# Performance work log

Hardware: AMD Instinct MI355X
Metric: run time of the kernel (lower is better)

The kernel has to match this reference:

```python
import jax, jax.numpy as jnp
import numpy as np

DIM = 1024
HEADS = 8
DIM_HEAD = 64
INNER = HEADS * DIM_HEAD  # 512
N_PATCHES = 256
SCALE = DIM_HEAD ** -0.5


def setup_inputs() -> dict:
    key = jax.random.key(0)
    ks = jax.random.split(key, 6)
    s = lambda fan_in: 1.0 / np.sqrt(fan_in)
    return {
        "x": jax.random.normal(ks[0], (64, N_PATCHES, DIM), dtype=jnp.float32),
        "Wq": jax.random.normal(ks[1], (DIM, INNER), dtype=jnp.float32) * s(DIM),
        "Wkv": jax.random.normal(ks[2], (DIM, 2 * INNER), dtype=jnp.float32) * s(DIM),
        "Wout": jax.random.normal(ks[3], (INNER, DIM), dtype=jnp.float32) * s(INNER),
        "bout": jax.random.normal(ks[4], (DIM,), dtype=jnp.float32) * 0.01,
        "Wspec": jax.random.normal(ks[5], (N_PATCHES, 3 * N_PATCHES), dtype=jnp.float32) * s(N_PATCHES),
    }


def reference(x, Wq, Wkv, Wout, bout, Wspec):
    b, n, d = x.shape
    # ---- spatial: single center-query attention ----
    x_center = x[:, n // 2, :]                      # [b, d]
    q = (x_center @ Wq).reshape(b, HEADS, DIM_HEAD)  # [b, h, dh]
    kv = x @ Wkv                                     # [b, n, 2*inner]
    k, v = jnp.split(kv, 2, axis=-1)
    k = k.reshape(b, n, HEADS, DIM_HEAD).transpose(0, 2, 1, 3)  # [b, h, n, dh]
    v = v.reshape(b, n, HEADS, DIM_HEAD).transpose(0, 2, 1, 3)
    logits = jnp.einsum('bhd,bhnd->bhn', q, k) * SCALE
    attn = jax.nn.softmax(logits, axis=-1)           # [b, h, n]
    out = jnp.einsum('bhn,bhnd->bhd', attn, v).reshape(b, INNER)
    # torch expands attn over n identical rows BEFORE to_out; the rows are
    # identical, so broadcasting the projected row is the same math.
    spatial = out @ Wout + bout                      # [b, d]
    spatial_out = jnp.broadcast_to(spatial[:, None, :], (b, n, d))
    # ---- spectral: attention over transposed (feature) axis ----
    x_t = x.transpose(0, 2, 1)                       # [b, d, n]
    qkv = x_t @ Wspec                                # [b, d, 3n]
    q_s, k_s, v_s = jnp.split(qkv, 3, axis=-1)       # v_s unused (as in source)
    spec_logits = jnp.einsum('bin,bjn->bij', q_s, k_s) * SCALE  # [b, d, d]
    spec_weights = jax.nn.softmax(spec_logits, axis=-1)
    return jnp.einsum('bnd,bde->bne', spatial_out, spec_weights)
```

## Files before the change

### kernel.cpp

```cpp
#include <hip/hip_runtime.h>
#include <hip/hip_bf16.h>
#include <cstdint>

typedef _Float16 f16;
typedef _Float16 half8 __attribute__((ext_vector_type(8)));
typedef float f32x4 __attribute__((ext_vector_type(4)));

#define SCALE 0.125f

#define GLL(src, dst) __builtin_amdgcn_global_load_lds( \
    (const __attribute__((address_space(1))) unsigned int*)(src), \
    (__attribute__((address_space(3))) unsigned int*)(dst), 16, 0, 0)

__global__ __launch_bounds__(256) void prep_xT(const float* __restrict__ x, f16* __restrict__ xT) {
  __shared__ f16 tile[32][33];
  int b = blockIdx.z, nt = blockIdx.y, dt = blockIdx.x;
  int c = threadIdx.x & 31, rp = threadIdx.x >> 5;
  const float* xb = x + ((size_t)b*256 + nt*32)*1024 + dt*32;
#pragma unroll
  for (int p = 0; p < 4; ++p) { int r = p*8 + rp; tile[r][c] = (f16)xb[(size_t)r*1024 + c]; }
  __syncthreads();
  f16* o = xT + ((size_t)b*1024 + dt*32)*256 + nt*32;
#pragma unroll
  for (int p = 0; p < 4; ++p) { int r = p*8 + rp; o[(size_t)r*256 + c] = tile[c][r]; }
}

__global__ __launch_bounds__(256) void prep_WspecT(const float* __restrict__ W, f16* __restrict__ Wt) {
  __shared__ float tile[32][33];
  int jt = blockIdx.x, ct = blockIdx.y;
  int c = threadIdx.x & 31, rp = threadIdx.x >> 5;
#pragma unroll
  for (int p = 0; p < 4; ++p) { int r = p*8+rp; tile[r][c] = W[(size_t)(ct*32 + r)*768 + jt*32 + c]; }
  __syncthreads();
#pragma unroll
  for (int p = 0; p < 4; ++p) { int r = p*8+rp; Wt[(size_t)(jt*32 + r)*256 + ct*32 + c] = (f16)tile[c][r]; }
}

template<int KSTEPS, int AST, int BST, int CST, bool SCALEQ>
__global__ __launch_bounds__(256) void gemm128(const f16* __restrict__ Ag, const f16* __restrict__ Bg,
                                               f16* __restrict__ Cg, size_t aB, size_t bB, size_t cB) {
  __shared__ f16 As[2][128*32];
  __shared__ f16 Bs[2][128*32];
  const f16* A = Ag + (size_t)blockIdx.z*aB;
  const f16* B = Bg + (size_t)blockIdx.z*bB;
  f16* C = Cg + (size_t)blockIdx.z*cB;
  int t = threadIdx.x, lane = t & 63, wave = t >> 6;
  int l15 = lane & 15, l4 = lane >> 4;
  int wm = wave & 1, wn = wave >> 1;
  size_t m0 = (size_t)blockIdx.x*128, n0 = (size_t)blockIdx.y*128;
  float cscale = (SCALEQ && n0 < 256) ? SCALE : 1.0f;
  f32x4 acc[4][4];
#pragma unroll
  for (int i=0;i<4;++i)
#pragma unroll
    for (int j=0;j<4;++j) acc[i][j] = (f32x4){0.f,0.f,0.f,0.f};
  int rowS[2], chS[2];
#pragma unroll
  for (int c=0;c<2;++c) {
    int slot = c*256 + t;
    rowS[c] = slot >> 2;
    chS[c]  = (slot & 3) ^ ((slot >> 3) & 3);
  }
  int pc = (l4 ^ ((l15 >> 1) & 3)) * 8;

  auto STAGE = [&](int buf, int ks) {
    int k0 = ks*32;
#pragma unroll
    for (int c=0;c<2;++c) {
      GLL(A + (m0 + rowS[c])*(size_t)AST + k0 + chS[c]*8, &As[buf][(c*256 + wave*64)*8]);
      GLL(B + (n0 + rowS[c])*(size_t)BST + k0 + chS[c]*8, &Bs[buf][(c*256 + wave*64)*8]);
    }
  };

  STAGE(0, 0);
#pragma unroll 2
  for (int ks = 0; ks < KSTEPS; ++ks) {
    int cur = ks & 1;
    if (ks + 1 < KSTEPS) {
      STAGE(cur ^ 1, ks + 1);
      asm volatile("s_waitcnt vmcnt(4)" ::: "memory");
    } else {
      asm volatile("s_waitcnt vmcnt(0)" ::: "memory");
    }
    __builtin_amdgcn_s_barrier();
    __builtin_amdgcn_sched_barrier(0);
    half8 a[4], bb[4];
    const f16* Af = &As[cur][(wm*64 + l15)*32 + pc];
    const f16* Bf = &Bs[cur][(wn*64 + l15)*32 + pc];
#pragma unroll
    for (int mi=0;mi<4;++mi) a[mi]  = *(const half8*)(Af + mi*16*32);
#pragma unroll
    for (int ni=0;ni<4;++ni) bb[ni] = *(const half8*)(Bf + ni*16*32);
    __builtin_amdgcn_s_setprio(1);
#pragma unroll
    for (int mi=0;mi<4;++mi)
#pragma unroll
      for (int ni=0;ni<4;++ni)
        acc[mi][ni] = __builtin_amdgcn_mfma_f32_16x16x32_f16(a[mi], bb[ni], acc[mi][ni], 0,0,0);
    __builtin_amdgcn_s_setprio(0);
    __builtin_amdgcn_sched_barrier(0);
    __builtin_amdgcn_s_barrier();
  }
#pragma unroll
  for (int mi=0;mi<4;++mi)
#pragma unroll
    for (int ni=0;ni<4;++ni)
#pragma unroll
      for (int j=0;j<4;++j) {
        size_t row = m0 + wm*64 + mi*16 + 4*l4 + j;
        size_t col = n0 + wn*64 + ni*16 + l15;
        C[row*CST + col] = (f16)(acc[mi][ni][j] * cscale);
      }
}

__global__ __launch_bounds__(256) void qk(const float* __restrict__ x, const float* __restrict__ Wq,
                                          float* __restrict__ qbuf) {
  int b = blockIdx.x, h = blockIdx.y;
  int t = threadIdx.x;
  __shared__ float xc[1024];
  __shared__ float part[4][64];
  const float* xcg = x + ((size_t)b*256 + 128)*1024;
#pragma unroll
  for (int i = 0; i < 4; ++i) xc[t + 256*i] = xcg[t + 256*i];
  __syncthreads();
  int d = t & 63, chunk = t >> 6;
  float s = 0.f;
  const float* wq = Wq + (size_t)(chunk*256)*512 + h*64 + d;
#pragma unroll 8
  for (int c = 0; c < 256; ++c) s += xc[chunk*256 + c] * wq[(size_t)c*512];
  part[chunk][d] = s;
  __syncthreads();
  if (t < 64) qbuf[(size_t)b*512 + h*64 + t] = part[0][t]+part[1][t]+part[2][t]+part[3][t];
}

__global__ __launch_bounds__(256) void uk(const float* __restrict__ Wkv, const float* __restrict__ qbuf,
                                          f16* __restrict__ u16) {
  int h = blockIdx.x, dc = blockIdx.y;
  int t = threadIdx.x;
  __shared__ float Wk[32][64];
  __shared__ float qT[64][65];
  {
    int j = t & 63, g = t >> 6;
#pragma unroll
    for (int rr = 0; rr < 8; ++rr) {
      int dd = g*8 + rr;
      Wk[dd][j] = Wkv[(size_t)(dc*32 + dd)*1024 + h*64 + j];
    }
#pragma unroll
    for (int rr = 0; rr < 16; ++rr) {
      int bb = g*16 + rr;
      qT[j][bb] = qbuf[(size_t)bb*512 + h*64 + j];
    }
  }
  __syncthreads();
  int b = t & 63, dq = t >> 6;
#pragma unroll
  for (int i = 0; i < 8; ++i) {
    int dd = dq*8 + i;
    float s = 0.f;
#pragma unroll 8
    for (int j = 0; j < 64; ++j) s += qT[j][b] * Wk[dd][j];
    u16[((size_t)b*16 + h)*1024 + dc*32 + dd] = (f16)s;
  }
}

__global__ __launch_bounds__(64) void lgk(const float* __restrict__ x, const f16* __restrict__ u16,
                                          float* __restrict__ logitbuf) {
  int mt = blockIdx.x, b = blockIdx.y;
  int lane = threadIdx.x, l15 = lane & 15, l4 = lane >> 4;
  const float* Ap = x + ((size_t)b*256 + mt*16 + l15)*1024 + 8*l4;
  const f16* Bp = u16 + ((size_t)b*16 + l15)*1024 + 8*l4;
  f32x4 acc = (f32x4){0.f,0.f,0.f,0.f};
#pragma unroll 8
  for (int ks = 0; ks < 32; ++ks) {
    f32x4 lo = *(const f32x4*)(Ap + ks*32);
    f32x4 hi = *(const f32x4*)(Ap + ks*32 + 4);
    half8 h;
    h[0]=(f16)lo[0]; h[1]=(f16)lo[1]; h[2]=(f16)lo[2]; h[3]=(f16)lo[3];
    h[4]=(f16)hi[0]; h[5]=(f16)hi[1]; h[6]=(f16)hi[2]; h[7]=(f16)hi[3];
    acc = __builtin_amdgcn_mfma_f32_16x16x32_f16(h, *(const half8*)(Bp + ks*32), acc, 0,0,0);
  }
  if (l15 < 8) {
#pragma unroll
    for (int j = 0; j < 4; ++j)
      logitbuf[((size_t)b*256 + mt*16 + 4*l4 + j)*8 + l15] = acc[j];
  }
}

__global__ __launch_bounds__(256) void sm(const float* __restrict__ logitbuf, f16* __restrict__ attnW) {
  int b = blockIdx.x, t = threadIdx.x;
  __shared__ float eL[256][9];
  __shared__ float Zs[8];
  float e[8];
  const float* lp = logitbuf + (size_t)b*256*8 + (size_t)t*8;
#pragma unroll
  for (int h = 0; h < 8; ++h) { e[h] = __expf(lp[h] * SCALE); eL[t][h] = e[h]; }
  __syncthreads();
  {
    int h = t >> 5, i = t & 31;
    float s = 0.f;
#pragma unroll
    for (int k = 0; k < 8; ++k) s += eL[i + 32*k][h];
#pragma unroll
    for (int o = 1; o < 32; o <<= 1) s += __shfl_xor(s, o);
    if (i == 0) Zs[h] = s;
  }
  __syncthreads();
#pragma unroll
  for (int h = 0; h < 8; ++h) attnW[((size_t)b*16 + h)*256 + t] = (f16)(e[h] / Zs[h]);
#pragma unroll
  for (int h = 8; h < 16; ++h) attnW[((size_t)b*16 + h)*256 + t] = (f16)0.f;
}

__global__ __launch_bounds__(64) void xbk(const f16* __restrict__ attnW, const f16* __restrict__ xT,
                                          f16* __restrict__ xbar) {
  int dt = blockIdx.x, b = blockIdx.y;
  int lane = threadIdx.x, l15 = lane & 15, l4 = lane >> 4;
  const f16* Ap = attnW + ((size_t)b*16 + l15)*256 + 8*l4;
  const f16* Bp = xT + ((size_t)b*1024 + dt*16 + l15)*256 + 8*l4;
  f32x4 acc = (f32x4){0.f,0.f,0.f,0.f};
#pragma unroll
  for (int ks = 0; ks < 8; ++ks)
    acc = __builtin_amdgcn_mfma_f32_16x16x32_f16(*(const half8*)(Ap + ks*32),
                                                 *(const half8*)(Bp + ks*32), acc, 0,0,0);
  if (l4 < 2) {
#pragma unroll
    for (int j = 0; j < 4; ++j)
      xbar[((size_t)b*8 + 4*l4 + j)*1024 + dt*16 + l15] = (f16)acc[j];
  }
}

__global__ __launch_bounds__(256) void vk(const f16* __restrict__ xbar, const float* __restrict__ Wkv,
                                          float* __restrict__ attnout) {
  int h = blockIdx.x, dc = blockIdx.y, bc = blockIdx.z;
  int t = threadIdx.x;
  __shared__ float Wv[256][64];
  {
    int j = t & 63, g = t >> 6;
#pragma unroll
    for (int rr = 0; rr < 64; ++rr) {
      int dd = g*64 + rr;
      Wv[dd][j] = Wkv[(size_t)(dc*256 + dd)*1024 + 512 + h*64 + j];
    }
  }
  __syncthreads();
  int j = t & 63, bq = t >> 6;
  float s[4] = {0.f,0.f,0.f,0.f};
  const f16* xp[4];
#pragma unroll
  for (int bl = 0; bl < 4; ++bl)
    xp[bl] = xbar + ((size_t)(bc*16 + bq*4 + bl)*8 + h)*1024 + dc*256;
  for (int d8 = 0; d8 < 32; ++d8) {
    half8 xv[4];
#pragma unroll
    for (int bl = 0; bl < 4; ++bl) xv[bl] = *(const half8*)(xp[bl] + d8*8);
#pragma unroll
    for (int i = 0; i < 8; ++i) {
      float w = Wv[d8*8 + i][j];
#pragma unroll
      for (int bl = 0; bl < 4; ++bl) s[bl] += (float)xv[bl][i] * w;
    }
  }
#pragma unroll
  for (int bl = 0; bl < 4; ++bl)
    atomicAdd(&attnout[(size_t)(bc*16 + bq*4 + bl)*512 + h*64 + j], s[bl]);
}

__global__ __launch_bounds__(256) void spatialp(const float* __restrict__ attnout, const float* __restrict__ Wout,
                                                float* __restrict__ partial) {
  int ic = blockIdx.x, b = blockIdx.y;
  int t = threadIdx.x;
  __shared__ float ao[128];
  if (t < 128) ao[t] = attnout[(size_t)b*512 + ic*128 + t];
  __syncthreads();
  const float* W = Wout + (size_t)ic*128*1024 + t*4;
  f32x4 acc0 = (f32x4){0.f,0.f,0.f,0.f};
  f32x4 acc1 = (f32x4){0.f,0.f,0.f,0.f};
#pragma unroll 4
  for (int i = 0; i < 128; i += 2) {
    f32x4 w0 = *(const f32x4*)(W + (size_t)i*1024);
    f32x4 w1 = *(const f32x4*)(W + (size_t)(i+1)*1024);
    float a0 = ao[i], a1 = ao[i+1];
    acc0[0] += a0*w0[0]; acc0[1] += a0*w0[1]; acc0[2] += a0*w0[2]; acc0[3] += a0*w0[3];
    acc1[0] += a1*w1[0]; acc1[1] += a1*w1[1]; acc1[2] += a1*w1[2]; acc1[3] += a1*w1[3];
  }
  f32x4 acc;
#pragma unroll
  for (int j=0;j<4;++j) acc[j] = acc0[j] + acc1[j];
  *(f32x4*)(partial + ((size_t)(b*4 + ic))*1024 + t*4) = acc;
}

__global__ __launch_bounds__(256) void spatialr(const float* __restrict__ partial, const float* __restrict__ bout,
                                                float* __restrict__ spatial) {
  int b = blockIdx.x, t = threadIdx.x;
  f32x4 s = *(const f32x4*)(bout + t*4);
#pragma unroll
  for (int ic = 0; ic < 4; ++ic) {
    f32x4 p = *(const f32x4*)(partial + ((size_t)(b*4 + ic))*1024 + t*4);
#pragma unroll
    for (int j=0;j<4;++j) s[j] += p[j];
  }
  *(f32x4*)(spatial + (size_t)b*1024 + t*4) = s;
}

__global__ __launch_bounds__(1024, 4) void speck(const f16* __restrict__ qks, const float* __restrict__ spatial,
                                                 float* __restrict__ r) {
  __shared__ f16 Bs[4][512*32];
  __shared__ f16 As[3][64*32];
  __shared__ __attribute__((aligned(16))) float sz[64*16];
  __shared__ float spat[64];
  __shared__ float zfin[64];
  int bid = blockIdx.x;
  int xcd = bid & 7, q = bid >> 3;
  int b = xcd*8 + (q >> 4);
  int iblk = q & 15;
  int t = threadIdx.x, lane = t & 63, wave = t >> 6;
  int l15 = lane & 15, l4 = lane >> 4;
  const f16* qs = qks + (size_t)b*1024*512;
  int i0 = iblk*64;
  if (t < 64) spat[t] = spatial[(size_t)b*1024 + i0 + t];

  f32x4 acc[4][4];
#pragma unroll
  for (int mi=0;mi<4;++mi)
#pragma unroll
    for (int ni=0;ni<4;++ni) acc[mi][ni] = (f32x4){0.f,0.f,0.f,0.f};
  int pc = (l4 ^ ((l15 >> 1) & 3)) * 8;

  auto STAGE = [&](int p) {
    int s = p & 3, hh = p & 1, ks = p >> 1;
    int k0 = ks*32;
#pragma unroll
    for (int c = 0; c < 2; ++c) {
      int u = c*1024 + t;
      int row = u >> 2;
      int ch = (u & 3) ^ ((u >> 3) & 3);
      GLL(qs + (size_t)(hh*512 + row)*512 + 256 + k0 + ch*8, &Bs[s][(c*1024 + wave*64)*8]);
    }
    if (hh == 0 && wave < 4) {
      int u = wave*64 + lane;
      int row = u >> 2;
      int ch = (u & 3) ^ ((u >> 3) & 3);
      GLL(qs + (size_t)(i0 + row)*512 + k0 + ch*8, &As[ks % 3][(wave*64)*8]);
    }
  };

  STAGE(0); STAGE(1); STAGE(2);
  half8 a[4];
#pragma unroll
  for (int p = 0; p < 16; ++p) {
    if (p < 14) {
      if (wave < 4) asm volatile("s_waitcnt vmcnt(5)" ::: "memory");
      else          asm volatile("s_waitcnt vmcnt(4)" ::: "memory");
    } else if (p == 14) {
      asm volatile("s_waitcnt vmcnt(2)" ::: "memory");
    } else {
      asm volatile("s_waitcnt vmcnt(0)" ::: "memory");
    }
    __builtin_amdgcn_s_barrier();
    __builtin_amdgcn_sched_barrier(0);
    if (p < 13) STAGE(p + 3);
    {
      int s = p & 3, hh = p & 1, sA = (p >> 1) % 3;
      if (hh == 0) {
#pragma unroll
        for (int mi = 0; mi < 4; ++mi)
          a[mi] = *(const half8*)(&As[sA][(mi*16 + l15)*32 + pc]);
      }
      __builtin_amdgcn_s_setprio(1);
#pragma unroll
      for (int c = 0; c < 2; ++c) {
        half8 bb = *(const half8*)(&Bs[s][(wave*32 + c*16 + l15)*32 + pc]);
#pragma unroll
        for (int mi = 0; mi < 4; ++mi)
          acc[mi][hh*2+c] = __builtin_amdgcn_mfma_f32_16x16x32_f16(a[mi], bb, acc[mi][hh*2+c], 0,0,0);
      }
      __builtin_amdgcn_s_setprio(0);
      __builtin_amdgcn_sched_barrier(0);
    }
  }
#pragma unroll
  for (int mi=0;mi<4;++mi)
#pragma unroll
    for (int jj=0;jj<4;++jj) {
      float s = 0.f;
#pragma unroll
      for (int ni=0;ni<4;++ni) {
        float e = __expf(acc[mi][ni][jj]);
        acc[mi][ni][jj] = e;
        s += e;
      }
#pragma unroll
      for (int o=1;o<16;o<<=1) s += __shfl_xor(s, o);
      if (l15 == 0) sz[(mi*16 + 4*l4 + jj)*16 + wave] = s;
    }
  __syncthreads();
  {
    float v = sz[t];
#pragma unroll
    for (int o=1;o<16;o<<=1) v += __shfl_xor(v, o);
    if ((t & 15) == 0) zfin[t >> 4] = v;
  }
  __syncthreads();
  float f[4][4];
#pragma unroll
  for (int mi=0;mi<4;++mi)
#pragma unroll
    for (int jj=0;jj<4;++jj) {
      int row = mi*16 + 4*l4 + jj;
      f[mi][jj] = spat[row] / zfin[row];
    }
  float* rb = r + (size_t)b*1024;
#pragma unroll
  for (int ni=0;ni<4;++ni) {
    float v = 0.f;
#pragma unroll
    for (int mi=0;mi<4;++mi)
#pragma unroll
      for (int jj=0;jj<4;++jj) v += f[mi][jj]*acc[mi][ni][jj];
    v += __shfl_xor(v, 16);
    v += __shfl_xor(v, 32);
    if (l4 == 0) atomicAdd(rb + (ni>>1)*512 + wave*32 + (ni&1)*16 + l15, v);
  }
}

__global__ __launch_bounds__(256) void bcast(const float* __restrict__ r, float* __restrict__ out) {
  size_t row = blockIdx.x;
  int b = (int)(row >> 8);
  f32x4 v = *(const f32x4*)(r + (size_t)b*1024 + threadIdx.x*4);
  *(f32x4*)(out + row*1024 + (size_t)threadIdx.x*4) = v;
}

extern "C" void kernel_launch(void* const* d_in, const int* in_sizes, int n_in,
                              void* d_out, int out_size, void* d_ws, size_t ws_size,
                              hipStream_t stream) {
  const float* x     = (const float*)d_in[0];
  const float* Wq    = (const float*)d_in[1];
  const float* Wkv   = (const float*)d_in[2];
  const float* Wout  = (const float*)d_in[3];
  const float* bout  = (const float*)d_in[4];
  const float* Wspec = (const float*)d_in[5];
  float* out = (float*)d_out;
  char* ws = (char*)d_ws;
  f16*   qks      = (f16*)(ws);
  f16*   u16pad   = (f16*)(ws);
  float* partial  = (float*)(ws);
  float* logitbuf = (float*)(ws + 2097152);
  f16*   attnW    = (f16*)(ws + 2621440);
  f16*   xbar     = (f16*)(ws + 3145728);
  float* qbuf     = (float*)(ws + 5242880);
  f16*   xT       = (f16*)(ws + 67108864);
  f16*   WspecT   = (f16*)(ws + 102760448);
  float* attnout  = (float*)(ws + 103022592);
  float* spatial  = (float*)(ws + 103153664);
  float* rvec     = (float*)(ws + 103415808);
  (void)in_sizes; (void)n_in; (void)out_size; (void)ws_size;

  prep_xT    <<<dim3(32, 8, 64), dim3(256), 0, stream>>>(x, xT);
  prep_WspecT<<<dim3(16, 8),     dim3(256), 0, stream>>>(Wspec, WspecT);
  hipMemsetAsync(u16pad, 0, 2097152, stream);
  hipMemsetAsync(attnout, 0, 64*512*sizeof(float), stream);
  qk         <<<dim3(64, 8),     dim3(256), 0, stream>>>(x, Wq, qbuf);
  uk         <<<dim3(8, 32),     dim3(256), 0, stream>>>(Wkv, qbuf, u16pad);
  lgk        <<<dim3(16, 64),    dim3(64),  0, stream>>>(x, u16pad, logitbuf);
  sm         <<<dim3(64),        dim3(256), 0, stream>>>(logitbuf, attnW);
  xbk        <<<dim3(64, 64),    dim3(64),  0, stream>>>(attnW, xT, xbar);
  vk         <<<dim3(8, 4, 4),   dim3(256), 0, stream>>>(xbar, Wkv, attnout);
  spatialp   <<<dim3(4, 64),     dim3(256), 0, stream>>>(attnout, Wout, partial);
  spatialr   <<<dim3(64),        dim3(256), 0, stream>>>(partial, bout, spatial);
  gemm128<8,256,256,512,true><<<dim3(8, 4, 64), dim3(256), 0, stream>>>(xT, WspecT, qks,
                                                                   (size_t)1024*256, 0, (size_t)1024*512);
  hipMemsetAsync(rvec, 0, 64*1024*sizeof(float), stream);
  speck      <<<dim3(1024),      dim3(1024), 0, stream>>>(qks, spatial, rvec);
  bcast      <<<dim3(16384),     dim3(256), 0, stream>>>(rvec, out);
}
```

Measured before the change: 223.4 us.

## Reassociate spectral logits through a precomputed Wq·Wkᵀ product

Rewrites the spectral logits q_s·k_sᵀ = xT·Wq_s·Wk_sᵀ·x as (xT·M)·x with M = Wq_s·Wk_sᵀ, computed once by a small GEMM. The per-batch GEMM then produces a 1024x256 Y instead of the 1024x512 q_s/k_s pair, and speck multiplies Y directly against xT. This halves the per-batch projection FLOPs and the intermediate traffic. speck is restructured around it: 512 threads, each wave owning 128 columns, A operands loaded straight into registers, B staged per-wave in LDS with double buffering, and a simpler row-sum reduction. The reassociation changes fp16 rounding order, which may shift accuracy.

```diff
diff --git a/kernel.cpp b/kernel.cpp
--- a/kernel.cpp
+++ b/kernel.cpp
@@ -11,6 +11,9 @@
 #define GLL(src, dst) __builtin_amdgcn_global_load_lds( \
     (const __attribute__((address_space(1))) unsigned int*)(src), \
     (__attribute__((address_space(3))) unsigned int*)(dst), 16, 0, 0)
+
+#define GLD(dst, addr) asm volatile("global_load_dwordx4 %0, %1, off" \
+    : "=&v"(dst) : "v"(addr) : "memory")
 
 __global__ __launch_bounds__(256) void prep_xT(const float* __restrict__ x, f16* __restrict__ xT) {
   __shared__ f16 tile[32][33];
@@ -25,15 +28,10 @@
   for (int p = 0; p < 4; ++p) { int r = p*8 + rp; o[(size_t)r*256 + c] = tile[c][r]; }
 }
 
-__global__ __launch_bounds__(256) void prep_WspecT(const float* __restrict__ W, f16* __restrict__ Wt) {
-  __shared__ float tile[32][33];
-  int jt = blockIdx.x, ct = blockIdx.y;
-  int c = threadIdx.x & 31, rp = threadIdx.x >> 5;
-#pragma unroll
-  for (int p = 0; p < 4; ++p) { int r = p*8+rp; tile[r][c] = W[(size_t)(ct*32 + r)*768 + jt*32 + c]; }
-  __syncthreads();
-#pragma unroll
-  for (int p = 0; p < 4; ++p) { int r = p*8+rp; Wt[(size_t)(jt*32 + r)*256 + ct*32 + c] = (f16)tile[c][r]; }
+__global__ __launch_bounds__(256) void prep_Wspec16(const float* __restrict__ W, f16* __restrict__ Wt) {
+  int row = blockIdx.x, t = threadIdx.x;
+  Wt[(size_t)row*512 + t]       = (f16)W[(size_t)row*768 + t];
+  Wt[(size_t)row*512 + 256 + t] = (f16)W[(size_t)row*768 + 256 + t];
 }
 
 template<int KSTEPS, int AST, int BST, int CST, bool SCALEQ>
@@ -48,7 +46,6 @@
   int l15 = lane & 15, l4 = lane >> 4;
   int wm = wave & 1, wn = wave >> 1;
   size_t m0 = (size_t)blockIdx.x*128, n0 = (size_t)blockIdx.y*128;
-  float cscale = (SCALEQ && n0 < 256) ? SCALE : 1.0f;
   f32x4 acc[4][4];
 #pragma unroll
   for (int i=0;i<4;++i)
@@ -101,6 +98,7 @@
     __builtin_amdgcn_sched_barrier(0);
     __builtin_amdgcn_s_barrier();
   }
+  float cscale = SCALEQ ? SCALE : 1.0f;
 #pragma unroll
   for (int mi=0;mi<4;++mi)
 #pragma unroll
@@ -303,81 +301,71 @@
   *(f32x4*)(spatial + (size_t)b*1024 + t*4) = s;
 }
 
-__global__ __launch_bounds__(1024, 4) void speck(const f16* __restrict__ qks, const float* __restrict__ spatial,
-                                                 float* __restrict__ r) {
-  __shared__ f16 Bs[4][512*32];
-  __shared__ f16 As[3][64*32];
-  __shared__ __attribute__((aligned(16))) float sz[64*16];
+__global__ __launch_bounds__(512, 2) void speck(const f16* __restrict__ Y, const f16* __restrict__ xT,
+                                                const float* __restrict__ spatial, float* __restrict__ r) {
+  __shared__ f16 Bs[8][2][128*32];
+  __shared__ __attribute__((aligned(16))) float sz[64*8];
   __shared__ float spat[64];
-  __shared__ float zfin[64];
   int bid = blockIdx.x;
   int xcd = bid & 7, q = bid >> 3;
   int b = xcd*8 + (q >> 4);
   int iblk = q & 15;
   int t = threadIdx.x, lane = t & 63, wave = t >> 6;
   int l15 = lane & 15, l4 = lane >> 4;
-  const f16* qs = qks + (size_t)b*1024*512;
+  const f16* Yb  = Y  + (size_t)b*262144;
+  const f16* xTb = xT + (size_t)b*262144;
   int i0 = iblk*64;
   if (t < 64) spat[t] = spatial[(size_t)b*1024 + i0 + t];
 
-  f32x4 acc[4][4];
+  f32x4 acc[4][8];
 #pragma unroll
   for (int mi=0;mi<4;++mi)
 #pragma unroll
-    for (int ni=0;ni<4;++ni) acc[mi][ni] = (f32x4){0.f,0.f,0.f,0.f};
+    for (int ni=0;ni<8;++ni) acc[mi][ni] = (f32x4){0.f,0.f,0.f,0.f};
   int pc = (l4 ^ ((l15 >> 1) & 3)) * 8;
-
-  auto STAGE = [&](int p) {
-    int s = p & 3, hh = p & 1, ks = p >> 1;
+  int rowB = lane >> 2;
+  int chB  = (lane & 3) ^ ((lane >> 3) & 3);
+
+  half8 a[3][4];
+
+  auto STAGE_B = [&](int ks) {
+    int slot = ks & 1, k0 = ks*32;
+#pragma unroll
+    for (int c = 0; c < 8; ++c) {
+      GLL(xTb + (size_t)(wave*128 + c*16 + rowB)*256 + k0 + chB*8,
+          &Bs[wave][slot][c*512]);
+    }
+  };
+  auto LOAD_A = [&](int ks, half8* dst) {
     int k0 = ks*32;
 #pragma unroll
-    for (int c = 0; c < 2; ++c) {
-      int u = c*1024 + t;
-      int row = u >> 2;
-      int ch = (u & 3) ^ ((u >> 3) & 3);
-      GLL(qs + (size_t)(hh*512 + row)*512 + 256 + k0 + ch*8, &Bs[s][(c*1024 + wave*64)*8]);
-    }
-    if (hh == 0 && wave < 4) {
-      int u = wave*64 + lane;
-      int row = u >> 2;
-      int ch = (u & 3) ^ ((u >> 3) & 3);
-      GLL(qs + (size_t)(i0 + row)*512 + k0 + ch*8, &As[ks % 3][(wave*64)*8]);
+    for (int mi = 0; mi < 4; ++mi) {
+      const f16* ap = Yb + (size_t)(i0 + mi*16 + l15)*256 + k0 + 8*l4;
+      GLD(dst[mi], ap);
     }
   };
 
-  STAGE(0); STAGE(1); STAGE(2);
-  half8 a[4];
-#pragma unroll
-  for (int p = 0; p < 16; ++p) {
-    if (p < 14) {
-      if (wave < 4) asm volatile("s_waitcnt vmcnt(5)" ::: "memory");
-      else          asm volatile("s_waitcnt vmcnt(4)" ::: "memory");
-    } else if (p == 14) {
-      asm volatile("s_waitcnt vmcnt(2)" ::: "memory");
-    } else {
-      asm volatile("s_waitcnt vmcnt(0)" ::: "memory");
-    }
-    __builtin_amdgcn_s_barrier();
+  LOAD_A(0, a[0]); STAGE_B(0); LOAD_A(1, a[1]); STAGE_B(1);
+#pragma unroll
+  for (int ks = 0; ks < 8; ++ks) {
+    if (ks < 7) asm volatile("s_waitcnt vmcnt(12)" ::: "memory");
+    else        asm volatile("s_waitcnt vmcnt(0)"  ::: "memory");
     __builtin_amdgcn_sched_barrier(0);
-    if (p < 13) STAGE(p + 3);
-    {
-      int s = p & 3, hh = p & 1, sA = (p >> 1) % 3;
-      if (hh == 0) {
-#pragma unroll
-        for (int mi = 0; mi < 4; ++mi)
-          a[mi] = *(const half8*)(&As[sA][(mi*16 + l15)*32 + pc]);
-      }
-      __builtin_amdgcn_s_setprio(1);
-#pragma unroll
-      for (int c = 0; c < 2; ++c) {
-        half8 bb = *(const half8*)(&Bs[s][(wave*32 + c*16 + l15)*32 + pc]);
-#pragma unroll
-        for (int mi = 0; mi < 4; ++mi)
-          acc[mi][hh*2+c] = __builtin_amdgcn_mfma_f32_16x16x32_f16(a[mi], bb, acc[mi][hh*2+c], 0,0,0);
-      }
-      __builtin_amdgcn_s_setprio(0);
-      __builtin_amdgcn_sched_barrier(0);
-    }
+    half8 bb[8];
+#pragma unroll
+    for (int ni = 0; ni < 8; ++ni)
+      bb[ni] = *(const half8*)(&Bs[wave][ks & 1][(ni*16 + l15)*32 + pc]);
+    asm volatile("s_waitcnt lgkmcnt(0)" ::: "memory");
+    __builtin_amdgcn_sched_barrier(0);
+    if (ks < 6) { LOAD_A(ks + 2, a[(ks + 2) % 3]); STAGE_B(ks + 2); }
+    __builtin_amdgcn_s_setprio(1);
+#pragma unroll
+    for (int ni = 0; ni < 8; ++ni)
+#pragma unroll
+      for (int mi = 0; mi < 4; ++mi)
+        acc[mi][ni] = __builtin_amdgcn_mfma_f32_16x16x32_f16(a[ks % 3][mi], bb[ni], acc[mi][ni], 0,0,0);
+    __builtin_amdgcn_s_setprio(0);
+    __builtin_amdgcn_sched_barrier(0);
   }
 #pragma unroll
   for (int mi=0;mi<4;++mi)
@@ -385,22 +373,15 @@
     for (int jj=0;jj<4;++jj) {
       float s = 0.f;
 #pragma unroll
-      for (int ni=0;ni<4;++ni) {
+      for (int ni=0;ni<8;++ni) {
         float e = __expf(acc[mi][ni][jj]);
         acc[mi][ni][jj] = e;
         s += e;
       }
 #pragma unroll
       for (int o=1;o<16;o<<=1) s += __shfl_xor(s, o);
-      if (l15 == 0) sz[(mi*16 + 4*l4 + jj)*16 + wave] = s;
-    }
-  __syncthreads();
-  {
-    float v = sz[t];
-#pragma unroll
-    for (int o=1;o<16;o<<=1) v += __shfl_xor(v, o);
-    if ((t & 15) == 0) zfin[t >> 4] = v;
-  }
+      if (l15 == 0) sz[(mi*16 + 4*l4 + jj)*8 + wave] = s;
+    }
   __syncthreads();
   float f[4][4];
 #pragma unroll
@@ -408,11 +389,14 @@
 #pragma unroll
     for (int jj=0;jj<4;++jj) {
       int row = mi*16 + 4*l4 + jj;
-      f[mi][jj] = spat[row] / zfin[row];
+      f32x4 lo = *(const f32x4*)(&sz[row*8]);
+      f32x4 hi = *(const f32x4*)(&sz[row*8+4]);
+      float zz = (lo[0]+lo[1]+lo[2]+lo[3]) + (hi[0]+hi[1]+hi[2]+hi[3]);
+      f[mi][jj] = spat[row] / zz;
     }
   float* rb = r + (size_t)b*1024;
 #pragma unroll
-  for (int ni=0;ni<4;++ni) {
+  for (int ni=0;ni<8;++ni) {
     float v = 0.f;
 #pragma unroll
     for (int mi=0;mi<4;++mi)
@@ -420,7 +404,7 @@
       for (int jj=0;jj<4;++jj) v += f[mi][jj]*acc[mi][ni][jj];
     v += __shfl_xor(v, 16);
     v += __shfl_xor(v, 32);
-    if (l4 == 0) atomicAdd(rb + (ni>>1)*512 + wave*32 + (ni&1)*16 + l15, v);
+    if (l4 == 0) atomicAdd(rb + wave*128 + ni*16 + l15, v);
   }
 }
 
@@ -442,35 +426,37 @@
   const float* Wspec = (const float*)d_in[5];
   float* out = (float*)d_out;
   char* ws = (char*)d_ws;
-  f16*   qks      = (f16*)(ws);
+  f16*   Ybuf     = (f16*)(ws);
   f16*   u16pad   = (f16*)(ws);
   float* partial  = (float*)(ws);
   float* logitbuf = (float*)(ws + 2097152);
   f16*   attnW    = (f16*)(ws + 2621440);
   f16*   xbar     = (f16*)(ws + 3145728);
   float* qbuf     = (float*)(ws + 5242880);
+  f16*   MT       = (f16*)(ws + 33554432);
   f16*   xT       = (f16*)(ws + 67108864);
-  f16*   WspecT   = (f16*)(ws + 102760448);
+  f16*   Wspec16  = (f16*)(ws + 102760448);
   float* attnout  = (float*)(ws + 103022592);
   float* spatial  = (float*)(ws + 103153664);
   float* rvec     = (float*)(ws + 103415808);
   (void)in_sizes; (void)n_in; (void)out_size; (void)ws_size;
 
-  prep_xT    <<<dim3(32, 8, 64), dim3(256), 0, stream>>>(x, xT);
-  prep_WspecT<<<dim3(16, 8),     dim3(256), 0, stream>>>(Wspec, WspecT);
+  prep_xT     <<<dim3(32, 8, 64), dim3(256), 0, stream>>>(x, xT);
+  prep_Wspec16<<<dim3(256),       dim3(256), 0, stream>>>(Wspec, Wspec16);
+  gemm128<8,512,512,256,false><<<dim3(2, 2, 1), dim3(256), 0, stream>>>(Wspec16 + 256, Wspec16, MT, 0, 0, 0);
   hipMemsetAsync(u16pad, 0, 2097152, stream);
   hipMemsetAsync(attnout, 0, 64*512*sizeof(float), stream);
-  qk         <<<dim3(64, 8),     dim3(256), 0, stream>>>(x, Wq, qbuf);
-  uk         <<<dim3(8, 32),     dim3(256), 0, stream>>>(Wkv, qbuf, u16pad);
-  lgk        <<<dim3(16, 64),    dim3(64),  0, stream>>>(x, u16pad, logitbuf);
-  sm         <<<dim3(64),        dim3(256), 0, stream>>>(logitbuf, attnW);
-  xbk        <<<dim3(64, 64),    dim3(64),  0, stream>>>(attnW, xT, xbar);
-  vk         <<<dim3(8, 4, 4),   dim3(256), 0, stream>>>(xbar, Wkv, attnout);
-  spatialp   <<<dim3(4, 64),     dim3(256), 0, stream>>>(attnout, Wout, partial);
-  spatialr   <<<dim3(64),        dim3(256), 0, stream>>>(partial, bout, spatial);
-  gemm128<8,256,256,512,true><<<dim3(8, 4, 64), dim3(256), 0, stream>>>(xT, WspecT, qks,
-                                                                   (size_t)1024*256, 0, (size_t)1024*512);
+  qk          <<<dim3(64, 8),     dim3(256), 0, stream>>>(x, Wq, qbuf);
+  uk          <<<dim3(8, 32),     dim3(256), 0, stream>>>(Wkv, qbuf, u16pad);
+  lgk         <<<dim3(16, 64),    dim3(64),  0, stream>>>(x, u16pad, logitbuf);
+  sm          <<<dim3(64),        dim3(256), 0, stream>>>(logitbuf, attnW);
+  xbk         <<<dim3(64, 64),    dim3(64),  0, stream>>>(attnW, xT, xbar);
+  vk          <<<dim3(8, 4, 4),   dim3(256), 0, stream>>>(xbar, Wkv, attnout);
+  spatialp    <<<dim3(4, 64),     dim3(256), 0, stream>>>(attnout, Wout, partial);
+  spatialr    <<<dim3(64),        dim3(256), 0, stream>>>(partial, bout, spatial);
+  gemm128<8,256,256,256,true><<<dim3(8, 2, 64), dim3(256), 0, stream>>>(xT, MT, Ybuf,
+                                                                        262144, 0, 262144);
   hipMemsetAsync(rvec, 0, 64*1024*sizeof(float), stream);
-  speck      <<<dim3(1024),      dim3(1024), 0, stream>>>(qks, spatial, rvec);
-  bcast      <<<dim3(16384),     dim3(256), 0, stream>>>(rvec, out);
-}
+  speck       <<<dim3(1024),      dim3(512), 0, stream>>>(Ybuf, xT, spatial, rvec);
+  bcast       <<<dim3(16384),     dim3(256), 0, stream>>>(rvec, out);
+}
```

Result: no change. 226.6 us (+1.5%).
